# Optimization experiments

Hardware: AMD Instinct MI355X
Metric: run time of the kernel (lower is better)

The kernel has to match this reference:

```python
import jax, jax.numpy as jnp
import numpy as np
from jax import lax

B, C_IN, L = 512, 32, 512
E = 8
POOL = 16            # AdaptiveAvgPool1d(16)
D_IN = C_IN * L      # expert input = flattened x
D_OUT = 768          # pooler_output dim (hard-coded in module)
TAU = 1.0            # gumbel temperature
BN_EPS = 1e-5


def setup_inputs() -> dict:
    key = jax.random.key(0)
    ks = jax.random.split(key, 8)
    s = 0.02
    return {
        "x": jax.random.normal(ks[0], (B, C_IN, L), jnp.float32),
        "gumbel_u": jax.random.uniform(ks[1], (B, E), jnp.float32, 1e-6, 1.0 - 1e-6),
        "conv_w": jax.random.normal(ks[2], (64, C_IN, 3), jnp.float32) * s,
        "conv_b": jnp.zeros((64,), jnp.float32),
        "bn_gamma": jnp.ones((64 * POOL,), jnp.float32),
        "bn_beta": jnp.zeros((64 * POOL,), jnp.float32),
        "bn_mean": jnp.zeros((64 * POOL,), jnp.float32),
        "bn_var": jnp.ones((64 * POOL,), jnp.float32),
        "fc1_w": jax.random.normal(ks[3], (128, 64 * POOL), jnp.float32) * s,
        "fc1_b": jnp.zeros((128,), jnp.float32),
        "fc2_w": jax.random.normal(ks[4], (E, 128), jnp.float32) * s,
        "fc2_b": jnp.zeros((E,), jnp.float32),
        "expert_w": jax.random.normal(ks[5], (E, D_IN, D_OUT), jnp.float32) * s,
        "expert_b": jnp.zeros((E, D_OUT), jnp.float32),
    }


def _gelu(v):
    return jax.nn.gelu(v, approximate=False)  # torch nn.GELU default (erf)


def reference(x, gumbel_u, conv_w, conv_b, bn_gamma, bn_beta, bn_mean, bn_var,
              fc1_w, fc1_b, fc2_w, fc2_b, expert_w, expert_b):
    # ---- router ----
    h = lax.conv_general_dilated(x, conv_w, (1,), ((1, 1),),
                                 dimension_numbers=("NCH", "OIH", "NCH"))
    h = _gelu(h + conv_b[None, :, None])                     # [B,64,L]
    h = h.reshape(B, 64, POOL, L // POOL).mean(-1)           # adaptive avg pool -> [B,64,16]
    h = h.reshape(B, 64 * POOL)                              # flatten
    h = (h - bn_mean) * lax.rsqrt(bn_var + BN_EPS) * bn_gamma + bn_beta  # BN (eval)
    h = _gelu(h @ fc1_w.T + fc1_b)                           # dropout inactive in eval
    logits = h @ fc2_w.T + fc2_b                             # [B,E]

    # ---- soft gumbel-softmax gating (hard=False), then top-2 ----
    g = -jnp.log(-jnp.log(gumbel_u))
    routing_weights = jax.nn.softmax((logits + g) / TAU, axis=1)
    topv, topi = lax.top_k(routing_weights, 2)               # [B,2]
    w = topv / (topv.sum(axis=1, keepdims=True) + 1e-8)      # [B,2]

    # ---- dispatch/compute/combine (dense-expert stand-in: flatten + linear) ----
    xf = x.reshape(B, D_IN)
    all_out = jnp.einsum("bd,edh->beh", xf, expert_w) + expert_b[None]  # [B,E,768]
    sel = jnp.take_along_axis(all_out, topi[:, :, None], axis=1)        # [B,2,768]
    pooler_output = (sel * w[:, :, None]).sum(axis=1)                   # [B,768]
    return pooler_output
```

## Files before the change

kernel.cpp:

```cpp
#include <hip/hip_runtime.h>
#include <hip/hip_bf16.h>

#define NB 512
#define CIN 32
#define LEN 512
#define NE 8
#define NPOOL 16
#define DIN 16384
#define DOUT 768
#define HD 1024
#define F1 128

#define MT 256
#define NT 128
#define BK 32
#define NBUF 4

typedef __attribute__((ext_vector_type(4))) float f32x4;
typedef __attribute__((ext_vector_type(8))) short s16x8;
typedef __attribute__((ext_vector_type(4))) unsigned int u32x4;

__device__ __forceinline__ float gelu_erf(float v) {
    return 0.5f * v * (1.0f + erff(v * 0.70710678118654752f));
}

__device__ __forceinline__ unsigned cvt_pk(float lo, float hi) {
    unsigned r;
    asm volatile("v_cvt_pk_bf16_f32 %0, %1, %2" : "=v"(r) : "v"(lo), "v"(hi));
    return r;
}

__device__ __forceinline__ unsigned short f2bf_u(float f) {
    union { float f; unsigned u; } x; x.f = f;
    unsigned r = x.u + 0x7fffu + ((x.u >> 16) & 1u);
    return (unsigned short)(r >> 16);
}

__device__ __forceinline__ void gload_lds16(const void* gptr, void* lptr) {
    __builtin_amdgcn_global_load_lds(
        (const __attribute__((address_space(1))) unsigned int*)gptr,
        (__attribute__((address_space(3))) unsigned int*)lptr,
        16, 0, 0);
}

__global__ __launch_bounds__(256) void kcvt(const float* __restrict__ x,
                                            unsigned short* __restrict__ xb)
{
    int i = blockIdx.x * 256 + threadIdx.x;
    const f32x4* src = (const f32x4*)(x + (size_t)i * 8);
    f32x4 v0 = src[0], v1 = src[1];
    u32x4 pk;
    pk[0] = cvt_pk(v0[0], v0[1]); pk[1] = cvt_pk(v0[2], v0[3]);
    pk[2] = cvt_pk(v1[0], v1[1]); pk[3] = cvt_pk(v1[2], v1[3]);
    *(u32x4*)(xb + (size_t)i * 8) = pk;
}

__global__ __launch_bounds__(256) void krouter_conv(
    const float* __restrict__ x, const float* __restrict__ cw, const float* __restrict__ cb,
    const float* __restrict__ bng, const float* __restrict__ bnb,
    const float* __restrict__ bnm, const float* __restrict__ bnv,
    float* __restrict__ h, int* __restrict__ cnt)
{
    __shared__ float xs[CIN * 264];
    int half = blockIdx.x;
    int b = blockIdx.y;
    int t = threadIdx.x;
    if (b == 0 && half == 0 && t < NE) cnt[t] = 0;

    int Lchunk0 = half * 64 - 1;
    const float* xb_ = x + (size_t)b * DIN;
    for (int idx = t; idx < CIN * 66; idx += 256) {
        int ci = idx / 66;
        int cc = idx - ci * 66;
        int gc = min(max(Lchunk0 + cc, 0), 127);
        f32x4 v = *(const f32x4*)(xb_ + ci * 512 + gc * 4);
        int byte = ci * 1056 + ((cc << 4) ^ (((cc >> 3) & 7) << 4));
        *(f32x4*)((char*)xs + byte) = v;
    }
    __syncthreads();

    int p  = t & 7;
    int pg = half * 8 + p;
    int cq = t >> 3;
    int co0 = cq * 2, co1 = co0 + 1;

    float sa[32], sb[32];
    #pragma unroll
    for (int i = 0; i < 32; ++i) { sa[i] = 0.f; sb[i] = 0.f; }

    for (int ci = 0; ci < CIN; ++ci) {
        float f[40];
        #pragma unroll
        for (int u = 0; u < 10; ++u) {
            int lc = p * 8 + u;
            int byte = ci * 1056 + ((lc << 4) ^ (((lc >> 3) & 7) << 4));
            f32x4 v = *(const f32x4*)((const char*)xs + byte);
            f[4*u+0] = v[0]; f[4*u+1] = v[1]; f[4*u+2] = v[2]; f[4*u+3] = v[3];
        }
        if (pg == 0)  f[3]  = 0.f;
        if (pg == 15) f[36] = 0.f;
        float wa0 = cw[co0*96 + ci*3 + 0], wa1 = cw[co0*96 + ci*3 + 1], wa2 = cw[co0*96 + ci*3 + 2];
        float wb0 = cw[co1*96 + ci*3 + 0], wb1 = cw[co1*96 + ci*3 + 1], wb2 = cw[co1*96 + ci*3 + 2];
        #pragma unroll
        for (int i = 0; i < 32; ++i) {
            sa[i] = fmaf(f[i+3], wa0, fmaf(f[i+4], wa1, fmaf(f[i+5], wa2, sa[i])));
            sb[i] = fmaf(f[i+3], wb0, fmaf(f[i+4], wb1, fmaf(f[i+5], wb2, sb[i])));
        }
    }

    float ba = cb[co0], bbv = cb[co1];
    float ma = 0.f, mb = 0.f;
    #pragma unroll
    for (int i = 0; i < 32; ++i) { ma += gelu_erf(sa[i] + ba); mb += gelu_erf(sb[i] + bbv); }
    ma *= (1.f / 32.f); mb *= (1.f / 32.f);

    int oa = co0 * NPOOL + pg, ob = co1 * NPOOL + pg;
    float ra = (ma - bnm[oa]) * rsqrtf(bnv[oa] + 1e-5f) * bng[oa] + bnb[oa];
    float rb = (mb - bnm[ob]) * rsqrtf(bnv[ob] + 1e-5f) * bng[ob] + bnb[ob];
    h[(size_t)b * HD + oa] = ra;
    h[(size_t)b * HD + ob] = rb;
}

__global__ __launch_bounds__(256) void krouter_fc(
    const float* __restrict__ h, const float* __restrict__ f1w, const float* __restrict__ f1b,
    const float* __restrict__ f2w, const float* __restrict__ f2b,
    const float* __restrict__ gu,
    int* __restrict__ top2e, float* __restrict__ top2w,
    int* __restrict__ cnt, int* __restrict__ rowlist, float* __restrict__ roww)
{
    __shared__ float hs[8 * HD];
    __shared__ float h1s[8 * F1];
    __shared__ float lg[8 * NE];

    int bb = blockIdx.x * 8;
    int t = threadIdx.x;

    const f32x4* hg = (const f32x4*)(h + (size_t)bb * HD);
    f32x4* hs4 = (f32x4*)hs;
    #pragma unroll
    for (int u = 0; u < 8; ++u) hs4[t + 256 * u] = hg[t + 256 * u];
    __syncthreads();

    int j = t & 127;
    int pr = t >> 7;
    float acc[4] = {0.f, 0.f, 0.f, 0.f};
    const f32x4* w4 = (const f32x4*)(f1w + (size_t)j * HD);
    for (int k4 = 0; k4 < 256; ++k4) {
        f32x4 w = w4[k4];
        #pragma unroll
        for (int g = 0; g < 4; ++g) {
            f32x4 hv = hs4[(pr * 4 + g) * 256 + k4];
            acc[g] += w[0]*hv[0] + w[1]*hv[1] + w[2]*hv[2] + w[3]*hv[3];
        }
    }
    float bj = f1b[j];
    #pragma unroll
    for (int g = 0; g < 4; ++g) h1s[(pr * 4 + g) * F1 + j] = gelu_erf(acc[g] + bj);
    __syncthreads();

    if (t < 64) {
        int bi = t >> 3, e = t & 7;
        float s = f2b[e];
        const float* w = f2w + e * F1;
        const float* hh = h1s + bi * F1;
        #pragma unroll 8
        for (int k = 0; k < F1; ++k) s += hh[k] * w[k];
        lg[bi * NE + e] = s;
    }
    __syncthreads();

    if (t < 8) {
        int bi = t; int b = bb + bi;
        float r[NE];
        float mx = -1e30f;
        #pragma unroll
        for (int e = 0; e < NE; ++e) {
            float g = -logf(-logf(gu[b * NE + e]));
            r[e] = lg[bi * NE + e] + g;
            mx = fmaxf(mx, r[e]);
        }
        float sum = 0.f;
        #pragma unroll
        for (int e = 0; e < NE; ++e) { r[e] = expf(r[e] - mx); sum += r[e]; }
        float inv = 1.f / sum;
        #pragma unroll
        for (int e = 0; e < NE; ++e) r[e] *= inv;
        int e0 = 0; float v0 = r[0];
        #pragma unroll
        for (int e = 1; e < NE; ++e) if (r[e] > v0) { v0 = r[e]; e0 = e; }
        int e1 = -1; float v1 = -1.f;
        #pragma unroll
        for (int e = 0; e < NE; ++e) { if (e == e0) continue; if (r[e] > v1) { v1 = r[e]; e1 = e; } }
        float den = v0 + v1 + 1e-8f;
        float w0 = v0 / den, w1 = v1 / den;
        top2e[b * 2 + 0] = e0; top2e[b * 2 + 1] = e1;
        top2w[b * 2 + 0] = w0; top2w[b * 2 + 1] = w1;
        int p0 = atomicAdd(&cnt[e0], 1);
        rowlist[e0 * NB + p0] = b * 2 + 0; roww[e0 * NB + p0] = w0;
        int p1 = atomicAdd(&cnt[e1], 1);
        rowlist[e1 * NB + p1] = b * 2 + 1; roww[e1 * NB + p1] = w1;
    }
}

__global__ __launch_bounds__(512, 2) void kgemm(
    const unsigned short* __restrict__ xb, const float* __restrict__ ew,
    const int* __restrict__ cnt, const int* __restrict__ rowlist, const float* __restrict__ roww,
    unsigned short* __restrict__ ypart, int nkc, int kch)
{
    int nwg = gridDim.x;
    int cpx = nwg >> 3;
    int wg = (blockIdx.x & 7) * cpx + (blockIdx.x >> 3);
    int nt = wg % 6;
    int kc = (wg / 6) % nkc;
    int e  = wg / (6 * nkc);
    int cn = cnt[e];
    if (cn <= 0) return;

    __shared__ __align__(16) char As[NBUF][MT * 64];
    __shared__ __align__(16) char Bs[NBUF][BK * NT * 4];

    int t = threadIdx.x;
    int wid = t >> 6, lane = t & 63;
    int wm = wid >> 1, wn = wid & 1;
    int g = lane >> 4;
    int NS = kch / BK;
    int k0 = kc * kch;

    const char* gB = (const char*)ew + (size_t)e * DIN * DOUT * 4
                   + (size_t)k0 * (DOUT * 4) + nt * NT * 4;
    int keyb = wid >> 1;
    int brow0 = wid * 4 + (lane >> 5);
    const char* gpB0 = gB + (size_t)brow0 * (DOUT * 4) + ((size_t)((lane & 31) ^ keyb) << 4);
    const char* gpB1 = gpB0 + 2 * (DOUT * 4);
    int ldsB0 = wid * 2048, ldsB1 = wid * 2048 + 1024;

    int keya = ((lane >> 2) ^ (lane >> 4)) & 3;
    int aq = (lane & 3) ^ keya;
    int ldsA0 = wid * 2048, ldsA1 = wid * 2048 + 1024;

    int af_off[4];
    #pragma unroll
    for (int mi = 0; mi < 4; ++mi) {
        int m = wm * 64 + mi * 16 + (lane & 15);
        int key = ((m & 3) ^ ((m >> 2) & 3));
        af_off[mi] = m * 64 + ((g ^ key) << 4);
    }
    int cb[4];
    #pragma unroll
    for (int ni = 0; ni < 4; ++ni) {
        int n = wn * 64 + ni * 16 + (lane & 15);
        cb[ni] = (((n >> 2) ^ g) << 4) + ((n & 3) << 2);
    }

    for (int row0 = 0; row0 < cn; row0 += MT) {
        int mloc = min(MT, cn - row0);
        bool wact = (wm * 64 < mloc);

        int r0 = wid * 32 + (lane >> 2);
        int r1 = r0 + 16;
        size_t ab0 = (size_t)(rowlist[e * NB + row0 + min(r0, mloc - 1)] >> 1) * (DIN * 2);
        size_t ab1 = (size_t)(rowlist[e * NB + row0 + min(r1, mloc - 1)] >> 1) * (DIN * 2);
        const char* gpA0 = (const char*)xb + ab0 + (size_t)k0 * 2 + (aq << 4);
        const char* gpA1 = (const char*)xb + ab1 + (size_t)k0 * 2 + (aq << 4);

        f32x4 acc[4][4];
        #pragma unroll
        for (int i = 0; i < 4; ++i)
            #pragma unroll
            for (int jj = 0; jj < 4; ++jj) acc[i][jj] = (f32x4){0.f, 0.f, 0.f, 0.f};

        auto stage = [&](int s) {
            int bi = s & (NBUF - 1);
            size_t bo = (size_t)s * (BK * DOUT * 4);
            gload_lds16(gpB0 + bo, (char*)Bs[bi] + ldsB0);
            gload_lds16(gpB1 + bo, (char*)Bs[bi] + ldsB1);
            size_t ao = (size_t)s * (BK * 2);
            gload_lds16(gpA0 + ao, (char*)As[bi] + ldsA0);
            gload_lds16(gpA1 + ao, (char*)As[bi] + ldsA1);
        };

        stage(0);
        if (1 < NS) stage(1);

        for (int s = 0; s < NS; ++s) {
            if (s + 2 < NS) stage(s + 2);
            __builtin_amdgcn_sched_barrier(0);
            if (s + 2 < NS)      asm volatile("s_waitcnt vmcnt(8)" ::: "memory");
            else if (s + 1 < NS) asm volatile("s_waitcnt vmcnt(4)" ::: "memory");
            else                 asm volatile("s_waitcnt vmcnt(0)" ::: "memory");
            __builtin_amdgcn_sched_barrier(0);
            __builtin_amdgcn_s_barrier();
            __builtin_amdgcn_sched_barrier(0);

            if (wact) {
                const char* Ab = As[s & (NBUF - 1)];
                const char* Bb = Bs[s & (NBUF - 1)];
                __builtin_amdgcn_s_setprio(1);
                s16x8 af[4];
                #pragma unroll
                for (int mi = 0; mi < 4; ++mi)
                    af[mi] = *(const s16x8*)(Ab + af_off[mi]);
                #pragma unroll
                for (int ni = 0; ni < 4; ++ni) {
                    float v[8];
                    #pragma unroll
                    for (int j = 0; j < 8; ++j)
                        v[j] = *(const float*)(Bb + g * 4096 + j * 512 + cb[ni]);
                    union { u32x4 u; s16x8 v8; } bf;
                    bf.u[0] = cvt_pk(v[0], v[1]); bf.u[1] = cvt_pk(v[2], v[3]);
                    bf.u[2] = cvt_pk(v[4], v[5]); bf.u[3] = cvt_pk(v[6], v[7]);
                    #pragma unroll
                    for (int mi = 0; mi < 4; ++mi)
                        acc[mi][ni] = __builtin_amdgcn_mfma_f32_16x16x32_bf16(af[mi], bf.v8, acc[mi][ni], 0, 0, 0);
                }
                __builtin_amdgcn_s_setprio(0);
            }
        }

        if (wact) {
            #pragma unroll
            for (int mi = 0; mi < 4; ++mi) {
                #pragma unroll
                for (int rg = 0; rg < 4; ++rg) {
                    int m = wm * 64 + mi * 16 + g * 4 + rg;
                    if (m < mloc) {
                        int ent = rowlist[e * NB + row0 + m];
                        float wgt = roww[e * NB + row0 + m];
                        int ob = ent >> 1, slot = ent & 1;
                        unsigned short* dst = ypart + ((size_t)(slot * nkc + kc) * NB + ob) * DOUT
                                            + nt * NT + wn * 64 + (lane & 15);
                        #pragma unroll
                        for (int ni = 0; ni < 4; ++ni)
                            dst[ni * 16] = f2bf_u(acc[mi][ni][rg] * wgt);
                    }
                }
            }
        }
        asm volatile("s_waitcnt vmcnt(0) lgkmcnt(0)" ::: "memory");
        __builtin_amdgcn_s_barrier();
    }
}

__global__ __launch_bounds__(256) void kcombine(
    const unsigned short* __restrict__ ypart,
    const int* __restrict__ top2e, const float* __restrict__ top2w,
    const float* __restrict__ eb, float* __restrict__ out, int nplanes)
{
    int b = blockIdx.y;
    int n = blockIdx.x * 256 + threadIdx.x;
    float s = 0.f;
    for (int p = 0; p < nplanes; ++p) {
        unsigned v = ypart[((size_t)p * NB + b) * DOUT + n];
        union { unsigned u; float f; } c; c.u = v << 16;
        s += c.f;
    }
    int e0 = top2e[b * 2], e1 = top2e[b * 2 + 1];
    float w0 = top2w[b * 2], w1 = top2w[b * 2 + 1];
    s += w0 * eb[e0 * DOUT + n] + w1 * eb[e1 * DOUT + n];
    out[(size_t)b * DOUT + n] = s;
}

extern "C" void kernel_launch(void* const* d_in, const int* in_sizes, int n_in,
                              void* d_out, int out_size, void* d_ws, size_t ws_size,
                              hipStream_t stream)
{
    const float* x   = (const float*)d_in[0];
    const float* gu  = (const float*)d_in[1];
    const float* cw  = (const float*)d_in[2];
    const float* cb  = (const float*)d_in[3];
    const float* bng = (const float*)d_in[4];
    const float* bnb = (const float*)d_in[5];
    const float* bnm = (const float*)d_in[6];
    const float* bnv = (const float*)d_in[7];
    const float* f1w = (const float*)d_in[8];
    const float* f1b = (const float*)d_in[9];
    const float* f2w = (const float*)d_in[10];
    const float* f2b = (const float*)d_in[11];
    const float* ew  = (const float*)d_in[12];
    const float* eb  = (const float*)d_in[13];

    int nkc = (ws_size >= (size_t)48 * 1024 * 1024) ? 16 : 8;
    int kch = DIN / nkc;

    char* ws = (char*)d_ws;
    size_t off = 0;
    float* h       = (float*)(ws + off); off += (size_t)NB * HD * 4;
    int*   top2e   = (int*)(ws + off);   off += (size_t)NB * 2 * 4;
    float* top2w   = (float*)(ws + off); off += (size_t)NB * 2 * 4;
    int*   cnt     = (int*)(ws + off);   off += 256;
    int*   rowlist = (int*)(ws + off);   off += (size_t)NE * NB * 4;
    float* roww    = (float*)(ws + off); off += (size_t)NE * NB * 4;
    unsigned short* xbuf = (unsigned short*)(ws + off);
    off += (size_t)NB * DIN * 2;
    unsigned short* ypart = (unsigned short*)(ws + off);
    off += (size_t)2 * nkc * NB * DOUT * 2;

    kcvt<<<NB * DIN / 8 / 256, 256, 0, stream>>>(x, xbuf);
    krouter_conv<<<dim3(2, NB), 256, 0, stream>>>(x, cw, cb, bng, bnb, bnm, bnv, h, cnt);
    krouter_fc<<<NB / 8, 256, 0, stream>>>(h, f1w, f1b, f2w, f2b, gu,
                                           top2e, top2w, cnt, rowlist, roww);
    kgemm<<<NE * nkc * 6, 512, 0, stream>>>(xbuf, ew, cnt, rowlist, roww, ypart, nkc, kch);
    kcombine<<<dim3(3, NB), 256, 0, stream>>>(ypart, top2e, top2w, eb, (float*)d_out, 2 * nkc);
}
```

Baseline: 253.4 us.

## Fuse x bf16 conversion into router conv and restage expert-weight B tiles

Removes the standalone fp32→bf16 conversion kernel for x by writing bf16 x from the router conv kernel while it already loads x into LDS. The GEMM B path switches from async global→LDS fp32 copies, converted on every LDS read, to register-staged global loads that are converted to bf16 once and stored in a swizzled bf16 LDS layout. This cuts LDS footprint and per-MFMA conversion work, with a 3-buffer A ring and a 2-buffer B ring. The router FC kernel is also split into blocks of 4 rows instead of 8 for more parallelism. The risk is that synchronous register loads of B are less latency tolerant than async LDS loads.

```diff
diff --git a/kernel.cpp b/kernel.cpp
--- a/kernel.cpp
+++ b/kernel.cpp
@@ -14,7 +14,6 @@
 #define MT 256
 #define NT 128
 #define BK 32
-#define NBUF 4
 
 typedef __attribute__((ext_vector_type(4))) float f32x4;
 typedef __attribute__((ext_vector_type(8))) short s16x8;
@@ -43,23 +42,11 @@
         16, 0, 0);
 }
 
-__global__ __launch_bounds__(256) void kcvt(const float* __restrict__ x,
-                                            unsigned short* __restrict__ xb)
-{
-    int i = blockIdx.x * 256 + threadIdx.x;
-    const f32x4* src = (const f32x4*)(x + (size_t)i * 8);
-    f32x4 v0 = src[0], v1 = src[1];
-    u32x4 pk;
-    pk[0] = cvt_pk(v0[0], v0[1]); pk[1] = cvt_pk(v0[2], v0[3]);
-    pk[2] = cvt_pk(v1[0], v1[1]); pk[3] = cvt_pk(v1[2], v1[3]);
-    *(u32x4*)(xb + (size_t)i * 8) = pk;
-}
-
 __global__ __launch_bounds__(256) void krouter_conv(
     const float* __restrict__ x, const float* __restrict__ cw, const float* __restrict__ cb,
     const float* __restrict__ bng, const float* __restrict__ bnb,
     const float* __restrict__ bnm, const float* __restrict__ bnv,
-    float* __restrict__ h, int* __restrict__ cnt)
+    float* __restrict__ h, int* __restrict__ cnt, unsigned short* __restrict__ xbuf)
 {
     __shared__ float xs[CIN * 264];
     int half = blockIdx.x;
@@ -76,6 +63,14 @@
         f32x4 v = *(const f32x4*)(xb_ + ci * 512 + gc * 4);
         int byte = ci * 1056 + ((cc << 4) ^ (((cc >> 3) & 7) << 4));
         *(f32x4*)((char*)xs + byte) = v;
+        if (cc >= 1 && cc <= 64) {
+            int gc2 = Lchunk0 + cc;
+            unsigned lo = cvt_pk(v[0], v[1]);
+            unsigned hi = cvt_pk(v[2], v[3]);
+            unsigned long long pk8 = ((unsigned long long)hi << 32) | lo;
+            *(unsigned long long*)((char*)xbuf
+                + ((size_t)b * DIN + ci * 512 + gc2 * 4) * 2) = pk8;
+        }
     }
     __syncthreads();
 
@@ -128,37 +123,37 @@
     int* __restrict__ top2e, float* __restrict__ top2w,
     int* __restrict__ cnt, int* __restrict__ rowlist, float* __restrict__ roww)
 {
-    __shared__ float hs[8 * HD];
-    __shared__ float h1s[8 * F1];
-    __shared__ float lg[8 * NE];
-
-    int bb = blockIdx.x * 8;
+    __shared__ float hs[4 * HD];
+    __shared__ float h1s[4 * F1];
+    __shared__ float lg[4 * NE];
+
+    int bb = blockIdx.x * 4;
     int t = threadIdx.x;
 
     const f32x4* hg = (const f32x4*)(h + (size_t)bb * HD);
     f32x4* hs4 = (f32x4*)hs;
     #pragma unroll
-    for (int u = 0; u < 8; ++u) hs4[t + 256 * u] = hg[t + 256 * u];
+    for (int u = 0; u < 4; ++u) hs4[t + 256 * u] = hg[t + 256 * u];
     __syncthreads();
 
     int j = t & 127;
     int pr = t >> 7;
-    float acc[4] = {0.f, 0.f, 0.f, 0.f};
+    float acc[2] = {0.f, 0.f};
     const f32x4* w4 = (const f32x4*)(f1w + (size_t)j * HD);
     for (int k4 = 0; k4 < 256; ++k4) {
         f32x4 w = w4[k4];
         #pragma unroll
-        for (int g = 0; g < 4; ++g) {
-            f32x4 hv = hs4[(pr * 4 + g) * 256 + k4];
+        for (int g = 0; g < 2; ++g) {
+            f32x4 hv = hs4[(pr * 2 + g) * 256 + k4];
             acc[g] += w[0]*hv[0] + w[1]*hv[1] + w[2]*hv[2] + w[3]*hv[3];
         }
     }
     float bj = f1b[j];
     #pragma unroll
-    for (int g = 0; g < 4; ++g) h1s[(pr * 4 + g) * F1 + j] = gelu_erf(acc[g] + bj);
+    for (int g = 0; g < 2; ++g) h1s[(pr * 2 + g) * F1 + j] = gelu_erf(acc[g] + bj);
     __syncthreads();
 
-    if (t < 64) {
+    if (t < 32) {
         int bi = t >> 3, e = t & 7;
         float s = f2b[e];
         const float* w = f2w + e * F1;
@@ -169,7 +164,7 @@
     }
     __syncthreads();
 
-    if (t < 8) {
+    if (t < 4) {
         int bi = t; int b = bb + bi;
         float r[NE];
         float mx = -1e30f;
@@ -216,8 +211,8 @@
     int cn = cnt[e];
     if (cn <= 0) return;
 
-    __shared__ __align__(16) char As[NBUF][MT * 64];
-    __shared__ __align__(16) char Bs[NBUF][BK * NT * 4];
+    __shared__ __align__(16) char As[3][MT * 64];
+    __shared__ __align__(16) char Bs[2][NT * 64];
 
     int t = threadIdx.x;
     int wid = t >> 6, lane = t & 63;
@@ -226,30 +221,26 @@
     int NS = kch / BK;
     int k0 = kc * kch;
 
-    const char* gB = (const char*)ew + (size_t)e * DIN * DOUT * 4
-                   + (size_t)k0 * (DOUT * 4) + nt * NT * 4;
-    int keyb = wid >> 1;
-    int brow0 = wid * 4 + (lane >> 5);
-    const char* gpB0 = gB + (size_t)brow0 * (DOUT * 4) + ((size_t)((lane & 31) ^ keyb) << 4);
-    const char* gpB1 = gpB0 + 2 * (DOUT * 4);
-    int ldsB0 = wid * 2048, ldsB1 = wid * 2048 + 1024;
+    int nl = t & 127, kg = t >> 7;
+    const char* gpB = (const char*)ew + (size_t)e * DIN * DOUT * 4
+                    + ((size_t)k0 + kg * 8) * (DOUT * 4) + (size_t)(nt * NT + nl) * 4;
+    int swn = (nl ^ (nl >> 2)) & 3;
+    int bwr_off = nl * 64 + ((kg ^ swn) << 4);
 
     int keya = ((lane >> 2) ^ (lane >> 4)) & 3;
     int aq = (lane & 3) ^ keya;
     int ldsA0 = wid * 2048, ldsA1 = wid * 2048 + 1024;
 
-    int af_off[4];
+    int af_off[4], bf_off[4];
     #pragma unroll
     for (int mi = 0; mi < 4; ++mi) {
         int m = wm * 64 + mi * 16 + (lane & 15);
-        int key = ((m & 3) ^ ((m >> 2) & 3));
-        af_off[mi] = m * 64 + ((g ^ key) << 4);
-    }
-    int cb[4];
+        af_off[mi] = m * 64 + ((g ^ ((m ^ (m >> 2)) & 3)) << 4);
+    }
     #pragma unroll
     for (int ni = 0; ni < 4; ++ni) {
         int n = wn * 64 + ni * 16 + (lane & 15);
-        cb[ni] = (((n >> 2) ^ g) << 4) + ((n & 3) << 2);
+        bf_off[ni] = n * 64 + ((g ^ ((n ^ (n >> 2)) & 3)) << 4);
     }
 
     for (int row0 = 0; row0 < cn; row0 += MT) {
@@ -258,10 +249,12 @@
 
         int r0 = wid * 32 + (lane >> 2);
         int r1 = r0 + 16;
-        size_t ab0 = (size_t)(rowlist[e * NB + row0 + min(r0, mloc - 1)] >> 1) * (DIN * 2);
-        size_t ab1 = (size_t)(rowlist[e * NB + row0 + min(r1, mloc - 1)] >> 1) * (DIN * 2);
+        size_t ab0 = (size_t)(rowlist[e * NB + row0 + min(r0, mloc - 1)] >> 1) * ((size_t)DIN * 2);
+        size_t ab1 = (size_t)(rowlist[e * NB + row0 + min(r1, mloc - 1)] >> 1) * ((size_t)DIN * 2);
         const char* gpA0 = (const char*)xb + ab0 + (size_t)k0 * 2 + (aq << 4);
         const char* gpA1 = (const char*)xb + ab1 + (size_t)k0 * 2 + (aq << 4);
+
+        char* Acur = As[0]; char* Anx1 = As[1]; char* Anx2 = As[2];
 
         f32x4 acc[4][4];
         #pragma unroll
@@ -269,53 +262,83 @@
             #pragma unroll
             for (int jj = 0; jj < 4; ++jj) acc[i][jj] = (f32x4){0.f, 0.f, 0.f, 0.f};
 
-        auto stage = [&](int s) {
-            int bi = s & (NBUF - 1);
-            size_t bo = (size_t)s * (BK * DOUT * 4);
-            gload_lds16(gpB0 + bo, (char*)Bs[bi] + ldsB0);
-            gload_lds16(gpB1 + bo, (char*)Bs[bi] + ldsB1);
-            size_t ao = (size_t)s * (BK * 2);
-            gload_lds16(gpA0 + ao, (char*)As[bi] + ldsA0);
-            gload_lds16(gpA1 + ao, (char*)As[bi] + ldsA1);
-        };
-
-        stage(0);
-        if (1 < NS) stage(1);
-
-        for (int s = 0; s < NS; ++s) {
-            if (s + 2 < NS) stage(s + 2);
-            __builtin_amdgcn_sched_barrier(0);
-            if (s + 2 < NS)      asm volatile("s_waitcnt vmcnt(8)" ::: "memory");
-            else if (s + 1 < NS) asm volatile("s_waitcnt vmcnt(4)" ::: "memory");
-            else                 asm volatile("s_waitcnt vmcnt(0)" ::: "memory");
-            __builtin_amdgcn_sched_barrier(0);
-            __builtin_amdgcn_s_barrier();
-            __builtin_amdgcn_sched_barrier(0);
-
-            if (wact) {
-                const char* Ab = As[s & (NBUF - 1)];
-                const char* Bb = Bs[s & (NBUF - 1)];
-                __builtin_amdgcn_s_setprio(1);
-                s16x8 af[4];
-                #pragma unroll
-                for (int mi = 0; mi < 4; ++mi)
-                    af[mi] = *(const s16x8*)(Ab + af_off[mi]);
-                #pragma unroll
-                for (int ni = 0; ni < 4; ++ni) {
-                    float v[8];
-                    #pragma unroll
-                    for (int j = 0; j < 8; ++j)
-                        v[j] = *(const float*)(Bb + g * 4096 + j * 512 + cb[ni]);
-                    union { u32x4 u; s16x8 v8; } bf;
-                    bf.u[0] = cvt_pk(v[0], v[1]); bf.u[1] = cvt_pk(v[2], v[3]);
-                    bf.u[2] = cvt_pk(v[4], v[5]); bf.u[3] = cvt_pk(v[6], v[7]);
-                    #pragma unroll
-                    for (int mi = 0; mi < 4; ++mi)
-                        acc[mi][ni] = __builtin_amdgcn_mfma_f32_16x16x32_bf16(af[mi], bf.v8, acc[mi][ni], 0, 0, 0);
-                }
-                __builtin_amdgcn_s_setprio(0);
-            }
-        }
+        float Bq0[8], Bq1[8];
+
+        gload_lds16(gpA0, Acur + ldsA0);
+        gload_lds16(gpA1, Acur + ldsA1);
+        #pragma unroll
+        for (int j = 0; j < 8; ++j) Bq0[j] = *(const float*)(gpB + j * (DOUT * 4));
+        gload_lds16(gpA0 + BK * 2, Anx1 + ldsA0);
+        gload_lds16(gpA1 + BK * 2, Anx1 + ldsA1);
+        #pragma unroll
+        for (int j = 0; j < 8; ++j)
+            Bq1[j] = *(const float*)(gpB + (size_t)(BK * DOUT * 4) + j * (DOUT * 4));
+        __builtin_amdgcn_sched_barrier(0);
+        asm volatile("s_waitcnt vmcnt(10)" ::: "memory");
+        __builtin_amdgcn_sched_barrier(0);
+        {
+            u32x4 pk;
+            pk[0] = cvt_pk(Bq0[0], Bq0[1]); pk[1] = cvt_pk(Bq0[2], Bq0[3]);
+            pk[2] = cvt_pk(Bq0[4], Bq0[5]); pk[3] = cvt_pk(Bq0[6], Bq0[7]);
+            *(u32x4*)(Bs[0] + bwr_off) = pk;
+        }
+        asm volatile("s_waitcnt lgkmcnt(0)" ::: "memory");
+        __builtin_amdgcn_sched_barrier(0);
+        __builtin_amdgcn_s_barrier();
+        __builtin_amdgcn_sched_barrier(0);
+
+#define GSTEP(S, BLD, BCV)                                                        \
+        {                                                                         \
+            int s_ = (S);                                                         \
+            if (s_ + 2 < NS) {                                                    \
+                size_t ao = (size_t)(s_ + 2) * (BK * 2);                          \
+                gload_lds16(gpA0 + ao, Anx2 + ldsA0);                             \
+                gload_lds16(gpA1 + ao, Anx2 + ldsA1);                             \
+                const char* bsrc = gpB + (size_t)(s_ + 2) * ((size_t)BK * DOUT * 4); \
+                _Pragma("unroll")                                                 \
+                for (int j = 0; j < 8; ++j)                                       \
+                    BLD[j] = *(const float*)(bsrc + j * (DOUT * 4));              \
+            }                                                                     \
+            __builtin_amdgcn_sched_barrier(0);                                    \
+            if (wact) {                                                           \
+                const char* Bb = Bs[s_ & 1];                                      \
+                __builtin_amdgcn_s_setprio(1);                                    \
+                s16x8 af[4];                                                      \
+                _Pragma("unroll")                                                 \
+                for (int mi = 0; mi < 4; ++mi)                                    \
+                    af[mi] = *(const s16x8*)(Acur + af_off[mi]);                  \
+                _Pragma("unroll")                                                 \
+                for (int ni = 0; ni < 4; ++ni) {                                  \
+                    s16x8 bf = *(const s16x8*)(Bb + bf_off[ni]);                  \
+                    _Pragma("unroll")                                             \
+                    for (int mi = 0; mi < 4; ++mi)                                \
+                        acc[mi][ni] = __builtin_amdgcn_mfma_f32_16x16x32_bf16(    \
+                            af[mi], bf, acc[mi][ni], 0, 0, 0);                    \
+                }                                                                 \
+                __builtin_amdgcn_s_setprio(0);                                    \
+            }                                                                     \
+            __builtin_amdgcn_sched_barrier(0);                                    \
+            if (s_ + 2 < NS)      asm volatile("s_waitcnt vmcnt(10)" ::: "memory"); \
+            else if (s_ + 1 < NS) asm volatile("s_waitcnt vmcnt(0)" ::: "memory"); \
+            __builtin_amdgcn_sched_barrier(0);                                    \
+            if (s_ + 1 < NS) {                                                    \
+                u32x4 pk;                                                         \
+                pk[0] = cvt_pk(BCV[0], BCV[1]); pk[1] = cvt_pk(BCV[2], BCV[3]);   \
+                pk[2] = cvt_pk(BCV[4], BCV[5]); pk[3] = cvt_pk(BCV[6], BCV[7]);   \
+                *(u32x4*)(Bs[(s_ + 1) & 1] + bwr_off) = pk;                       \
+            }                                                                     \
+            asm volatile("s_waitcnt lgkmcnt(0)" ::: "memory");                    \
+            __builtin_amdgcn_sched_barrier(0);                                    \
+            __builtin_amdgcn_s_barrier();                                         \
+            __builtin_amdgcn_sched_barrier(0);                                    \
+            { char* tmp_ = Acur; Acur = Anx1; Anx1 = Anx2; Anx2 = tmp_; }         \
+        }
+
+        for (int s = 0; s < NS; s += 2) {
+            GSTEP(s, Bq0, Bq1);
+            GSTEP(s + 1, Bq1, Bq0);
+        }
+#undef GSTEP
 
         if (wact) {
             #pragma unroll
@@ -395,9 +418,8 @@
     unsigned short* ypart = (unsigned short*)(ws + off);
     off += (size_t)2 * nkc * NB * DOUT * 2;
 
-    kcvt<<<NB * DIN / 8 / 256, 256, 0, stream>>>(x, xbuf);
-    krouter_conv<<<dim3(2, NB), 256, 0, stream>>>(x, cw, cb, bng, bnb, bnm, bnv, h, cnt);
-    krouter_fc<<<NB / 8, 256, 0, stream>>>(h, f1w, f1b, f2w, f2b, gu,
+    krouter_conv<<<dim3(2, NB), 256, 0, stream>>>(x, cw, cb, bng, bnb, bnm, bnv, h, cnt, xbuf);
+    krouter_fc<<<NB / 4, 256, 0, stream>>>(h, f1w, f1b, f2w, f2b, gu,
                                            top2e, top2w, cnt, rowlist, roww);
     kgemm<<<NE * nkc * 6, 512, 0, stream>>>(xbuf, ew, cnt, rowlist, roww, ypart, nkc, kch);
     kcombine<<<dim3(3, NB), 256, 0, stream>>>(ypart, top2e, top2w, eb, (float*)d_out, 2 * nkc);
```

After: 265.8 us. 4.9% more time.
